# Kernel optimization log

Hardware: AMD Instinct MI355X
Metric: run time of the kernel (lower is better)

The kernel has to match this reference:

```python
import jax, jax.numpy as jnp
import numpy as np

B = 4; E_PER = 100_000; E = B * E_PER
N_NODES = 50_000; N_REL = 500; D = 64; D_LG = 256
K_PER_VI = 20; S_VI = E // K_PER_VI          # 20000 sorted vi segments
S_VJ_PER = 5_000; S_VJ = B * S_VJ_PER        # 20000 unsorted vj segments
N_MEM = 131_072
INTERACT = ((0, 3), (0, 2, 3), (0, 4), (0, 2, 4), (1, 3), (1, 2, 3), (1, 4), (1, 2, 4))


def _build_edges():
    rng = np.random.default_rng(0)
    idx_vi = np.repeat(np.arange(S_VI), K_PER_VI)          # sorted segment ids
    gpb = S_VI // B
    eg = idx_vi // gpb                                     # sorted by eg_idx too
    vi = rng.integers(0, N_NODES, S_VI)[idx_vi]
    idx_vj = np.empty(E, dtype=np.int64)
    for b in range(B):
        loc = np.concatenate([np.arange(S_VJ_PER), rng.integers(0, S_VJ_PER, E_PER - S_VJ_PER)])
        rng.shuffle(loc)
        idx_vj[b * E_PER:(b + 1) * E_PER] = b * S_VJ_PER + loc  # every group non-empty
    vj = rng.integers(0, N_NODES, S_VJ)[idx_vj]            # consistent (eg, vj) per group
    rel = rng.integers(0, N_REL, E)
    e2vi = rng.integers(0, N_MEM, E)
    e2vj = rng.integers(0, N_MEM, E)
    return np.stack([eg, vi, vj, rel, idx_vi, idx_vj, e2vi, e2vj], axis=1).astype(np.int32)


def setup_inputs() -> dict:
    key = jax.random.key(0)
    ks = jax.random.split(key, 10)
    return {
        "node_attention": jax.random.uniform(ks[0], (B, N_NODES), jnp.float32),
        "scanned_edges": jnp.asarray(_build_edges()),
        "edges_y": jax.random.uniform(ks[1], (E,), jnp.float32),
        "hidden_uncon": jax.random.normal(ks[2], (1, N_NODES, D_LG), jnp.float32),
        "hidden_con": jax.random.normal(ks[3], (N_MEM, D), jnp.float32),
        "Wc": jax.random.normal(ks[4], (D, D), jnp.float32) / np.sqrt(D).astype(np.float32),
        "bc": jnp.zeros((D,), jnp.float32),
        "Wu": jax.random.normal(ks[5], (D_LG, D), jnp.float32) / np.sqrt(D_LG).astype(np.float32),
        "bu": jnp.zeros((D,), jnp.float32),
        "rel_table": jax.random.normal(ks[6], (N_REL, D), jnp.float32) * 0.05,
        "ws": jax.random.normal(ks[7], (len(INTERACT), D), jnp.float32) / np.sqrt(float(len(INTERACT))).astype(np.float32) if False else jax.random.normal(ks[7], (len(INTERACT), D), jnp.float32) * (1.0 / np.sqrt(len(INTERACT)).astype(np.float32)),
        "fb": jnp.zeros((D,), jnp.float32),
        "out_w": jax.random.normal(ks[8], (D,), jnp.float32),
        "out_b": jnp.zeros((D,), jnp.float32),
        "n_vi_segments": S_VI,
        "n_vj_segments": S_VJ,
    }


def reference(node_attention, scanned_edges, edges_y, hidden_uncon, hidden_con,
              Wc, bc, Wu, bu, rel_table, ws, fb, out_w, out_b,
              n_vi_segments, n_vj_segments):
    eg, vi, vj, rel = (scanned_edges[:, i] for i in range(4))
    idx_vi, idx_vj, e2vi, e2vj = (scanned_edges[:, i] for i in range(4, 8))
    # projections (proj_con / proj_uncon, tanh Dense)
    hc = jnp.tanh(hidden_con @ Wc + bc)          # [N_MEM, D]
    hu = jnp.tanh(hidden_uncon @ Wu + bu)[0]     # [n_nodes, D]; batch_size==1 path of Node2Edge
    # Node2Edge gathers
    feats = (hc[e2vi], hu[vi], rel_table[rel], hc[e2vj], hu[vj])  # each [E, D]
    # F layer: weighted sum of elementwise interaction products
    out = fb
    for k, idxs in enumerate(INTERACT):
        x = feats[idxs[0]]
        for i in idxs[1:]:
            x = x * feats[i]
        out = out + x * ws[k]
    out = jax.nn.relu(out) * out_w + out_b
    logits = jnp.sum(out, axis=1)                # [E]
    # NeighborSoftmax at 'vi' (sorted segment softmax)
    m = jax.ops.segment_max(logits, idx_vi, num_segments=n_vi_segments)
    ex = jnp.exp(logits - m[idx_vi])
    den = jax.ops.segment_sum(ex, idx_vi, num_segments=n_vi_segments)
    transition = ex / den[idx_vi]
    # attention flow: gather source attention, weight, aggregate at vj
    trans_att = transition * node_attention[eg, vi] * edges_y
    aggr = jax.ops.segment_sum(trans_att, idx_vj, num_segments=n_vj_segments)
    b_g = jax.ops.segment_max(eg, idx_vj, num_segments=n_vj_segments)
    vj_g = jax.ops.segment_max(vj, idx_vj, num_segments=n_vj_segments)
    new_node_attention = jnp.zeros_like(node_attention).at[b_g, vj_g].add(aggr)
    return new_node_attention
```

## Files before the change

### kernel.cpp

```cpp
#include <hip/hip_runtime.h>
#include <hip/hip_bf16.h>
#include <type_traits>

#define D 64
#define KPER 20

typedef __attribute__((ext_vector_type(8))) short short8;
typedef __attribute__((ext_vector_type(4))) float floatx4;

__device__ __forceinline__ unsigned short f2bfu(float x) {
    __hip_bfloat16 h = __float2bfloat16(x);
    return *reinterpret_cast<unsigned short*>(&h);
}
__device__ __forceinline__ float bfu2f(unsigned short u) {
    return __uint_as_float(((unsigned)u) << 16);
}

__device__ __forceinline__ float fast_tanh(float x) {
    float xc = fminf(fmaxf(x, -15.f), 15.f);
    float e = __expf(2.f * xc);
    return 1.f - 2.f * __builtin_amdgcn_rcpf(1.f + e);
}

template<int CTRL>
__device__ __forceinline__ float dpp_add(float x) {
    int t = __builtin_amdgcn_update_dpp(0, __float_as_int(x), CTRL, 0xf, 0xf, true);
    return x + __int_as_float(t);
}
template<int CTRL>
__device__ __forceinline__ float dpp_max(float x) {
    int xi = __float_as_int(x);
    int t = __builtin_amdgcn_update_dpp(xi, xi, CTRL, 0xf, 0xf, false);
    return fmaxf(x, __int_as_float(t));
}
__device__ __forceinline__ float wave_sum_b(float x) {
    x = dpp_add<0x111>(x); x = dpp_add<0x112>(x);
    x = dpp_add<0x114>(x); x = dpp_add<0x118>(x);
    x = dpp_add<0x142>(x); x = dpp_add<0x143>(x);
    return __int_as_float(__builtin_amdgcn_readlane(__float_as_int(x), 63));
}
__device__ __forceinline__ float wave_max_b(float x) {
    x = dpp_max<0x111>(x); x = dpp_max<0x112>(x);
    x = dpp_max<0x114>(x); x = dpp_max<0x118>(x);
    x = dpp_max<0x142>(x); x = dpp_max<0x143>(x);
    return __int_as_float(__builtin_amdgcn_readlane(__float_as_int(x), 63));
}

template<int I, int N, typename F>
__device__ __forceinline__ void static_for(F&& f) {
    if constexpr (I < N) {
        f(std::integral_constant<int, I>{});
        static_for<I + 1, N>(f);
    }
}

template<int SLOT>
__device__ __forceinline__ int get_slot(int m0, int m1, int m2) {
    if constexpr (SLOT < 64)       return __builtin_amdgcn_readlane(m0, SLOT);
    else if constexpr (SLOT < 128) return __builtin_amdgcn_readlane(m1, SLOT - 64);
    else                           return __builtin_amdgcn_readlane(m2, SLOT - 128);
}

__device__ __forceinline__ void proj64_pair(const float* __restrict__ h,
        const float* __restrict__ W, const float* __restrict__ b,
        unsigned short* __restrict__ out, int rt0) {
    constexpr int K = 64, KT = 2, CTN = 4;
    int lane = threadIdx.x & 63;
    int m = lane & 15, quad = lane >> 4;
    short8 bfr[CTN][KT];
    #pragma unroll
    for (int ct = 0; ct < CTN; ++ct)
        #pragma unroll
        for (int kt = 0; kt < KT; ++kt)
            #pragma unroll
            for (int j = 0; j < 8; ++j)
                bfr[ct][kt][j] = (short)f2bfu(W[(size_t)(kt * 32 + quad * 8 + j) * 64 + ct * 16 + m]);
    float bv[CTN];
    #pragma unroll
    for (int ct = 0; ct < CTN; ++ct) bv[ct] = b[ct * 16 + m];
    int rt1 = rt0 + 1;
    const float* hrow0 = h + (size_t)(rt0 * 16 + m) * K + quad * 8;
    const float* hrow1 = h + (size_t)(rt1 * 16 + m) * K + quad * 8;
    floatx4 a0[KT][2], a1[KT][2];
    #pragma unroll
    for (int kt = 0; kt < KT; ++kt) {
        a0[kt][0] = *(const floatx4*)(hrow0 + kt * 32);
        a0[kt][1] = *(const floatx4*)(hrow0 + kt * 32 + 4);
        a1[kt][0] = *(const floatx4*)(hrow1 + kt * 32);
        a1[kt][1] = *(const floatx4*)(hrow1 + kt * 32 + 4);
    }
    #pragma unroll
    for (int t = 0; t < 2; ++t) {
        floatx4 (*ar)[2] = t ? a1 : a0;
        int rt = t ? rt1 : rt0;
        floatx4 acc[CTN];
        #pragma unroll
        for (int ct = 0; ct < CTN; ++ct) acc[ct] = floatx4{0.f, 0.f, 0.f, 0.f};
        #pragma unroll
        for (int kt = 0; kt < KT; ++kt) {
            short8 af;
            #pragma unroll
            for (int j = 0; j < 4; ++j) {
                af[j]     = (short)f2bfu(ar[kt][0][j]);
                af[j + 4] = (short)f2bfu(ar[kt][1][j]);
            }
            #pragma unroll
            for (int ct = 0; ct < CTN; ++ct)
                acc[ct] = __builtin_amdgcn_mfma_f32_16x16x32_bf16(af, bfr[ct][kt], acc[ct], 0, 0, 0);
        }
        #pragma unroll
        for (int ct = 0; ct < CTN; ++ct) {
            int col = ct * 16 + m;
            #pragma unroll
            for (int reg = 0; reg < 4; ++reg) {
                int row = rt * 16 + quad * 4 + reg;
                out[(size_t)row * 64 + col] = f2bfu(fast_tanh(acc[ct][reg] + bv[ct]));
            }
        }
    }
}

__device__ __forceinline__ void proj256_body(const float* __restrict__ h,
        const float* __restrict__ W, const float* __restrict__ b,
        unsigned short* __restrict__ out, int ct0, int rt0, int rtstride, int ntiles) {
    constexpr int K = 256, KT = 8, CTN = 2;
    int lane = threadIdx.x & 63;
    int m = lane & 15, quad = lane >> 4;
    short8 bfr[CTN][KT];
    #pragma unroll
    for (int ct = 0; ct < CTN; ++ct)
        #pragma unroll
        for (int kt = 0; kt < KT; ++kt)
            #pragma unroll
            for (int j = 0; j < 8; ++j)
                bfr[ct][kt][j] = (short)f2bfu(W[(size_t)(kt * 32 + quad * 8 + j) * 64 + (ct0 + ct) * 16 + m]);
    float bv[CTN];
    #pragma unroll
    for (int ct = 0; ct < CTN; ++ct) bv[ct] = b[(ct0 + ct) * 16 + m];
    for (int rt = rt0; rt < ntiles; rt += rtstride) {
        floatx4 acc[CTN];
        #pragma unroll
        for (int ct = 0; ct < CTN; ++ct) acc[ct] = floatx4{0.f, 0.f, 0.f, 0.f};
        const float* hrow = h + (size_t)(rt * 16 + m) * K + quad * 8;
        #pragma unroll
        for (int kt = 0; kt < KT; ++kt) {
            floatx4 v0 = *(const floatx4*)(hrow + kt * 32);
            floatx4 v1 = *(const floatx4*)(hrow + kt * 32 + 4);
            short8 af;
            #pragma unroll
            for (int j = 0; j < 4; ++j) {
                af[j]     = (short)f2bfu(v0[j]);
                af[j + 4] = (short)f2bfu(v1[j]);
            }
            #pragma unroll
            for (int ct = 0; ct < CTN; ++ct)
                acc[ct] = __builtin_amdgcn_mfma_f32_16x16x32_bf16(af, bfr[ct][kt], acc[ct], 0, 0, 0);
        }
        #pragma unroll
        for (int ct = 0; ct < CTN; ++ct) {
            int col = (ct0 + ct) * 16 + m;
            #pragma unroll
            for (int reg = 0; reg < 4; ++reg) {
                int row = rt * 16 + quad * 4 + reg;
                out[(size_t)row * 64 + col] = f2bfu(fast_tanh(acc[ct][reg] + bv[ct]));
            }
        }
    }
}

#define RELB 16
#define ZB 8
__global__ __launch_bounds__(256) void proj_fused(
        const float* __restrict__ hcon, const float* __restrict__ Wc, const float* __restrict__ bc,
        const float* __restrict__ hun, const float* __restrict__ Wu, const float* __restrict__ bu,
        const float* __restrict__ relf, unsigned short* __restrict__ hc,
        unsigned short* __restrict__ hu, unsigned short* __restrict__ relb,
        float* __restrict__ outz, int nout,
        int t64, int t256, int g64, int g256, int nrel) {
    int bid = blockIdx.x;
    int w = threadIdx.x >> 6;
    if (bid < g64) {
        int wid = bid * 4 + w;
        proj64_pair(hcon, Wc, bc, hc, wid * 2);
    } else if (bid < g64 + g256) {
        int wid = (bid - g64) * 4 + w;
        int half = wid & 1;
        proj256_body(hun, Wu, bu, hu, half * 2, wid >> 1, (g256 * 4) >> 1, t256);
    } else if (bid < g64 + g256 + RELB) {
        int tid = (bid - g64 - g256) * 256 + threadIdx.x;
        for (int i = tid; i < nrel; i += RELB * 256) relb[i] = f2bfu(relf[i]);
    } else {
        int tid = (bid - g64 - g256 - RELB) * 256 + threadIdx.x;
        for (int i = tid; i < nout; i += ZB * 256) outz[i] = 0.0f;
    }
}

__global__ __launch_bounds__(256) void edge_kernel(
        const float* __restrict__ natt, const int* __restrict__ edges,
        const float* __restrict__ ey, const unsigned short* __restrict__ hc,
        const unsigned short* __restrict__ hu, const unsigned short* __restrict__ relt,
        const float* __restrict__ wsm, const float* __restrict__ fb,
        const float* __restrict__ outw, float* __restrict__ out, int N) {
    int lane = threadIdx.x & 63;
    int s = blockIdx.x * 4 + (threadIdx.x >> 6);
    long base = (long)s * KPER;
    const int* eb = edges + base * 8;
    int m0 = eb[lane];
    int m1 = eb[64 + lane];
    int m2 = (lane < 32) ? eb[128 + lane] : 0;
    int eg = get_slot<0>(m0, m1, m2);
    int vi = get_slot<1>(m0, m1, m2);
    float f1 = bfu2f(hu[(size_t)vi * D + lane]);
    float na = natt[(size_t)eg * N + vi];
    float w0 = wsm[0 * D + lane], w1 = wsm[1 * D + lane];
    float w2 = wsm[2 * D + lane], w3 = wsm[3 * D + lane];
    float w4 = wsm[4 * D + lane], w5 = wsm[5 * D + lane];
    float w6 = wsm[6 * D + lane], w7 = wsm[7 * D + lane];
    float fbv = fb[lane], owv = outw[lane];
    float myl = -INFINITY;
    int myvj = 0;
    static_for<0, KPER>([&](auto ec) {
        constexpr int e = decltype(ec)::value;
        int vj  = get_slot<e * 8 + 2>(m0, m1, m2);
        int rel = get_slot<e * 8 + 3>(m0, m1, m2);
        int evi = get_slot<e * 8 + 6>(m0, m1, m2);
        int evj = get_slot<e * 8 + 7>(m0, m1, m2);
        float F0 = bfu2f(hc[(size_t)evi * D + lane]);
        float F2 = bfu2f(relt[(size_t)rel * D + lane]);
        float F3 = bfu2f(hc[(size_t)evj * D + lane]);
        float F4 = bfu2f(hu[(size_t)vj * D + lane]);
        float t1 = fmaf(F2, w1, w0);
        float t2 = fmaf(F2, w5, w4);
        float t3 = fmaf(F2, w3, w2);
        float t4 = fmaf(F2, w7, w6);
        float u = fmaf(F0, t1, f1 * t2);
        float v = fmaf(F0, t3, f1 * t4);
        float o = fmaf(F3, u, fmaf(F4, v, fbv));
        o = fmaxf(o, 0.0f) * owv;
        float tot = wave_sum_b(o);
        bool mine = (lane == e);
        myl = mine ? tot : myl;
        myvj = mine ? vj : myvj;
    });
    float mx = wave_max_b(myl);
    float ex = __expf(myl - mx);
    float den = wave_sum_b(ex);
    if (lane < KPER) {
        float t = (ex / den) * na * ey[base + lane];
        atomicAdd(out + (size_t)eg * N + myvj, t);
    }
}

extern "C" void kernel_launch(void* const* d_in, const int* in_sizes, int n_in,
                              void* d_out, int out_size, void* d_ws, size_t ws_size,
                              hipStream_t stream) {
    const float* natt = (const float*)d_in[0];
    const int*   edges = (const int*)d_in[1];
    const float* ey   = (const float*)d_in[2];
    const float* hun  = (const float*)d_in[3];
    const float* hcon = (const float*)d_in[4];
    const float* Wc   = (const float*)d_in[5];
    const float* bc   = (const float*)d_in[6];
    const float* Wu   = (const float*)d_in[7];
    const float* bu   = (const float*)d_in[8];
    const float* relt = (const float*)d_in[9];
    const float* wsm  = (const float*)d_in[10];
    const float* fb   = (const float*)d_in[11];
    const float* outw = (const float*)d_in[12];
    float* out = (float*)d_out;

    int E    = in_sizes[2];
    int S    = E / KPER;
    int nmem = in_sizes[4] / D;
    int N    = in_sizes[3] / 256;
    int nrel = in_sizes[9];

    int t64  = nmem / 16;
    int t256 = N / 16;
    int g64  = t64 / 8;
    int g256 = 512;

    unsigned short* hc = (unsigned short*)d_ws;
    unsigned short* hu = hc + (size_t)nmem * D;
    unsigned short* rb = hu + (size_t)N * D;

    proj_fused<<<g64 + g256 + RELB + ZB, 256, 0, stream>>>(hcon, Wc, bc, hun, Wu, bu,
                                                           relt, hc, hu, rb,
                                                           out, out_size,
                                                           t64, t256, g64, g256, nrel);
    edge_kernel<<<S / 4, 256, 0, stream>>>(natt, edges, ey, hc, hu, rb,
                                           wsm, fb, outw, out, N);
}
```

Measured before the change: 209.2 us.

## Prefetch all edge gathers before compute and widen projection work per wave

The edge kernel now issues all 80 bf16 gathers for a segment's 20 edges up front into register arrays, before the compute and reduction loop. This exposes more memory-level parallelism instead of relying on the compiler to interleave loads with the cross-lane reductions. The 64-wide projection now does four row tiles per wave instead of two, and the 256-wide projection makes each wave cover all four column tiles rather than half. Both changes cut redundant weight loading and conversion, at the cost of higher register pressure and possibly lower occupancy.

```diff
diff --git a/kernel.cpp b/kernel.cpp
--- a/kernel.cpp
+++ b/kernel.cpp
@@ -61,10 +61,10 @@
     else                           return __builtin_amdgcn_readlane(m2, SLOT - 128);
 }
 
-__device__ __forceinline__ void proj64_pair(const float* __restrict__ h,
+__device__ __forceinline__ void proj64_quad(const float* __restrict__ h,
         const float* __restrict__ W, const float* __restrict__ b,
         unsigned short* __restrict__ out, int rt0) {
-    constexpr int K = 64, KT = 2, CTN = 4;
+    constexpr int K = 64, KT = 2, CTN = 4, NT = 4;
     int lane = threadIdx.x & 63;
     int m = lane & 15, quad = lane >> 4;
     short8 bfr[CTN][KT];
@@ -78,21 +78,19 @@
     float bv[CTN];
     #pragma unroll
     for (int ct = 0; ct < CTN; ++ct) bv[ct] = b[ct * 16 + m];
-    int rt1 = rt0 + 1;
-    const float* hrow0 = h + (size_t)(rt0 * 16 + m) * K + quad * 8;
-    const float* hrow1 = h + (size_t)(rt1 * 16 + m) * K + quad * 8;
-    floatx4 a0[KT][2], a1[KT][2];
-    #pragma unroll
-    for (int kt = 0; kt < KT; ++kt) {
-        a0[kt][0] = *(const floatx4*)(hrow0 + kt * 32);
-        a0[kt][1] = *(const floatx4*)(hrow0 + kt * 32 + 4);
-        a1[kt][0] = *(const floatx4*)(hrow1 + kt * 32);
-        a1[kt][1] = *(const floatx4*)(hrow1 + kt * 32 + 4);
-    }
-    #pragma unroll
-    for (int t = 0; t < 2; ++t) {
-        floatx4 (*ar)[2] = t ? a1 : a0;
-        int rt = t ? rt1 : rt0;
+    floatx4 a[NT][KT][2];
+    #pragma unroll
+    for (int t = 0; t < NT; ++t) {
+        const float* hrow = h + (size_t)((rt0 + t) * 16 + m) * K + quad * 8;
+        #pragma unroll
+        for (int kt = 0; kt < KT; ++kt) {
+            a[t][kt][0] = *(const floatx4*)(hrow + kt * 32);
+            a[t][kt][1] = *(const floatx4*)(hrow + kt * 32 + 4);
+        }
+    }
+    #pragma unroll
+    for (int t = 0; t < NT; ++t) {
+        int rt = rt0 + t;
         floatx4 acc[CTN];
         #pragma unroll
         for (int ct = 0; ct < CTN; ++ct) acc[ct] = floatx4{0.f, 0.f, 0.f, 0.f};
@@ -101,8 +99,8 @@
             short8 af;
             #pragma unroll
             for (int j = 0; j < 4; ++j) {
-                af[j]     = (short)f2bfu(ar[kt][0][j]);
-                af[j + 4] = (short)f2bfu(ar[kt][1][j]);
+                af[j]     = (short)f2bfu(a[t][kt][0][j]);
+                af[j + 4] = (short)f2bfu(a[t][kt][1][j]);
             }
             #pragma unroll
             for (int ct = 0; ct < CTN; ++ct)
@@ -120,10 +118,10 @@
     }
 }
 
-__device__ __forceinline__ void proj256_body(const float* __restrict__ h,
+__device__ __forceinline__ void proj256_full(const float* __restrict__ h,
         const float* __restrict__ W, const float* __restrict__ b,
-        unsigned short* __restrict__ out, int ct0, int rt0, int rtstride, int ntiles) {
-    constexpr int K = 256, KT = 8, CTN = 2;
+        unsigned short* __restrict__ out, int rt0, int rtstride, int ntiles) {
+    constexpr int K = 256, KT = 8, CTN = 4;
     int lane = threadIdx.x & 63;
     int m = lane & 15, quad = lane >> 4;
     short8 bfr[CTN][KT];
@@ -133,10 +131,10 @@
         for (int kt = 0; kt < KT; ++kt)
             #pragma unroll
             for (int j = 0; j < 8; ++j)
-                bfr[ct][kt][j] = (short)f2bfu(W[(size_t)(kt * 32 + quad * 8 + j) * 64 + (ct0 + ct) * 16 + m]);
+                bfr[ct][kt][j] = (short)f2bfu(W[(size_t)(kt * 32 + quad * 8 + j) * 64 + ct * 16 + m]);
     float bv[CTN];
     #pragma unroll
-    for (int ct = 0; ct < CTN; ++ct) bv[ct] = b[(ct0 + ct) * 16 + m];
+    for (int ct = 0; ct < CTN; ++ct) bv[ct] = b[ct * 16 + m];
     for (int rt = rt0; rt < ntiles; rt += rtstride) {
         floatx4 acc[CTN];
         #pragma unroll
@@ -158,7 +156,7 @@
         }
         #pragma unroll
         for (int ct = 0; ct < CTN; ++ct) {
-            int col = (ct0 + ct) * 16 + m;
+            int col = ct * 16 + m;
             #pragma unroll
             for (int reg = 0; reg < 4; ++reg) {
                 int row = rt * 16 + quad * 4 + reg;
@@ -181,11 +179,10 @@
     int w = threadIdx.x >> 6;
     if (bid < g64) {
         int wid = bid * 4 + w;
-        proj64_pair(hcon, Wc, bc, hc, wid * 2);
+        proj64_quad(hcon, Wc, bc, hc, wid * 4);
     } else if (bid < g64 + g256) {
         int wid = (bid - g64) * 4 + w;
-        int half = wid & 1;
-        proj256_body(hun, Wu, bu, hu, half * 2, wid >> 1, (g256 * 4) >> 1, t256);
+        proj256_full(hun, Wu, bu, hu, wid, g256 * 4, t256);
     } else if (bid < g64 + g256 + RELB) {
         int tid = (bid - g64 - g256) * 256 + threadIdx.x;
         for (int i = tid; i < nrel; i += RELB * 256) relb[i] = f2bfu(relf[i]);
@@ -212,6 +209,22 @@
     int vi = get_slot<1>(m0, m1, m2);
     float f1 = bfu2f(hu[(size_t)vi * D + lane]);
     float na = natt[(size_t)eg * N + vi];
+
+    unsigned short F0r[KPER], F2r[KPER], F3r[KPER], F4r[KPER];
+    int vjr[KPER];
+    static_for<0, KPER>([&](auto ec) {
+        constexpr int e = decltype(ec)::value;
+        int vj  = get_slot<e * 8 + 2>(m0, m1, m2);
+        int rel = get_slot<e * 8 + 3>(m0, m1, m2);
+        int evi = get_slot<e * 8 + 6>(m0, m1, m2);
+        int evj = get_slot<e * 8 + 7>(m0, m1, m2);
+        F0r[e] = hc[(size_t)evi * D + lane];
+        F2r[e] = relt[(size_t)rel * D + lane];
+        F3r[e] = hc[(size_t)evj * D + lane];
+        F4r[e] = hu[(size_t)vj * D + lane];
+        vjr[e] = vj;
+    });
+
     float w0 = wsm[0 * D + lane], w1 = wsm[1 * D + lane];
     float w2 = wsm[2 * D + lane], w3 = wsm[3 * D + lane];
     float w4 = wsm[4 * D + lane], w5 = wsm[5 * D + lane];
@@ -221,14 +234,10 @@
     int myvj = 0;
     static_for<0, KPER>([&](auto ec) {
         constexpr int e = decltype(ec)::value;
-        int vj  = get_slot<e * 8 + 2>(m0, m1, m2);
-        int rel = get_slot<e * 8 + 3>(m0, m1, m2);
-        int evi = get_slot<e * 8 + 6>(m0, m1, m2);
-        int evj = get_slot<e * 8 + 7>(m0, m1, m2);
-        float F0 = bfu2f(hc[(size_t)evi * D + lane]);
-        float F2 = bfu2f(relt[(size_t)rel * D + lane]);
-        float F3 = bfu2f(hc[(size_t)evj * D + lane]);
-        float F4 = bfu2f(hu[(size_t)vj * D + lane]);
+        float F0 = bfu2f(F0r[e]);
+        float F2 = bfu2f(F2r[e]);
+        float F3 = bfu2f(F3r[e]);
+        float F4 = bfu2f(F4r[e]);
         float t1 = fmaf(F2, w1, w0);
         float t2 = fmaf(F2, w5, w4);
         float t3 = fmaf(F2, w3, w2);
@@ -240,7 +249,7 @@
         float tot = wave_sum_b(o);
         bool mine = (lane == e);
         myl = mine ? tot : myl;
-        myvj = mine ? vj : myvj;
+        myvj = mine ? vjr[e] : myvj;
     });
     float mx = wave_max_b(myl);
     float ex = __expf(myl - mx);
@@ -277,7 +286,7 @@
 
     int t64  = nmem / 16;
     int t256 = N / 16;
-    int g64  = t64 / 8;
+    int g64  = t64 / 16;
     int g256 = 512;
 
     unsigned short* hc = (unsigned short*)d_ws;
```

Result: faster. 204.5 us (-2.2%).

## Process four edges per wave with vectorized bf16 gathers issued up front

Applied to the files above, without the earlier changes.

The edge kernel now splits each wave into four 16-lane groups. Each group handles one edge per iteration, with each lane owning 4 features loaded as a uint2 (4 bf16 values). All 20 edges' index loads and feature gathers are issued before any compute, which raises memory-level parallelism. Per-edge reductions shrink from 20 full-wave DPP reductions to 5 row-of-16 reductions plus a shuffle, and the per-edge readlane index extraction is replaced by direct per-group loads. The cost is higher register pressure from holding all gathered data at once.

```diff
diff --git a/kernel.cpp b/kernel.cpp
--- a/kernel.cpp
+++ b/kernel.cpp
@@ -45,20 +45,10 @@
     x = dpp_max<0x142>(x); x = dpp_max<0x143>(x);
     return __int_as_float(__builtin_amdgcn_readlane(__float_as_int(x), 63));
 }
-
-template<int I, int N, typename F>
-__device__ __forceinline__ void static_for(F&& f) {
-    if constexpr (I < N) {
-        f(std::integral_constant<int, I>{});
-        static_for<I + 1, N>(f);
-    }
-}
-
-template<int SLOT>
-__device__ __forceinline__ int get_slot(int m0, int m1, int m2) {
-    if constexpr (SLOT < 64)       return __builtin_amdgcn_readlane(m0, SLOT);
-    else if constexpr (SLOT < 128) return __builtin_amdgcn_readlane(m1, SLOT - 64);
-    else                           return __builtin_amdgcn_readlane(m2, SLOT - 128);
+__device__ __forceinline__ float row16_sum(float x) {
+    x = dpp_add<0x111>(x); x = dpp_add<0x112>(x);
+    x = dpp_add<0x114>(x); x = dpp_add<0x118>(x);
+    return x;
 }
 
 __device__ __forceinline__ void proj64_pair(const float* __restrict__ h,
@@ -195,6 +185,13 @@
     }
 }
 
+__device__ __forceinline__ void unp4(uint2 u, float f[4]) {
+    f[0] = __uint_as_float(u.x << 16);
+    f[1] = __uint_as_float(u.x & 0xffff0000u);
+    f[2] = __uint_as_float(u.y << 16);
+    f[3] = __uint_as_float(u.y & 0xffff0000u);
+}
+
 __global__ __launch_bounds__(256) void edge_kernel(
         const float* __restrict__ natt, const int* __restrict__ edges,
         const float* __restrict__ ey, const unsigned short* __restrict__ hc,
@@ -202,50 +199,68 @@
         const float* __restrict__ wsm, const float* __restrict__ fb,
         const float* __restrict__ outw, float* __restrict__ out, int N) {
     int lane = threadIdx.x & 63;
+    int g = lane >> 4, sub = lane & 15;
+    int l2 = lane >> 2;
     int s = blockIdx.x * 4 + (threadIdx.x >> 6);
     long base = (long)s * KPER;
     const int* eb = edges + base * 8;
-    int m0 = eb[lane];
-    int m1 = eb[64 + lane];
-    int m2 = (lane < 32) ? eb[128 + lane] : 0;
-    int eg = get_slot<0>(m0, m1, m2);
-    int vi = get_slot<1>(m0, m1, m2);
-    float f1 = bfu2f(hu[(size_t)vi * D + lane]);
+    int eg = __builtin_amdgcn_readfirstlane(eb[0]);
+    int vi = __builtin_amdgcn_readfirstlane(eb[1]);
+
+    const int* ebg = eb + g * 8;
+    int vjx[5], relx[5], evix[5], evjx[5];
+    #pragma unroll
+    for (int i = 0; i < 5; ++i) {
+        vjx[i]  = ebg[i * 32 + 2];
+        relx[i] = ebg[i * 32 + 3];
+        evix[i] = ebg[i * 32 + 6];
+        evjx[i] = ebg[i * 32 + 7];
+    }
+    uint2 G0[5], G2[5], G3[5], G4[5];
+    #pragma unroll
+    for (int i = 0; i < 5; ++i) {
+        G0[i] = *(const uint2*)(hc   + (size_t)evix[i] * D + sub * 4);
+        G2[i] = *(const uint2*)(relt + (size_t)relx[i] * D + sub * 4);
+        G3[i] = *(const uint2*)(hc   + (size_t)evjx[i] * D + sub * 4);
+        G4[i] = *(const uint2*)(hu   + (size_t)vjx[i]  * D + sub * 4);
+    }
+    uint2 F1u = *(const uint2*)(hu + (size_t)vi * D + sub * 4);
+    float f1[4];
+    unp4(F1u, f1);
+
+    floatx4 wv[8];
+    #pragma unroll
+    for (int k = 0; k < 8; ++k) wv[k] = *(const floatx4*)(wsm + k * D + sub * 4);
+    floatx4 fbv = *(const floatx4*)(fb + sub * 4);
+    floatx4 owv = *(const floatx4*)(outw + sub * 4);
     float na = natt[(size_t)eg * N + vi];
-    float w0 = wsm[0 * D + lane], w1 = wsm[1 * D + lane];
-    float w2 = wsm[2 * D + lane], w3 = wsm[3 * D + lane];
-    float w4 = wsm[4 * D + lane], w5 = wsm[5 * D + lane];
-    float w6 = wsm[6 * D + lane], w7 = wsm[7 * D + lane];
-    float fbv = fb[lane], owv = outw[lane];
+
     float myl = -INFINITY;
-    int myvj = 0;
-    static_for<0, KPER>([&](auto ec) {
-        constexpr int e = decltype(ec)::value;
-        int vj  = get_slot<e * 8 + 2>(m0, m1, m2);
-        int rel = get_slot<e * 8 + 3>(m0, m1, m2);
-        int evi = get_slot<e * 8 + 6>(m0, m1, m2);
-        int evj = get_slot<e * 8 + 7>(m0, m1, m2);
-        float F0 = bfu2f(hc[(size_t)evi * D + lane]);
-        float F2 = bfu2f(relt[(size_t)rel * D + lane]);
-        float F3 = bfu2f(hc[(size_t)evj * D + lane]);
-        float F4 = bfu2f(hu[(size_t)vj * D + lane]);
-        float t1 = fmaf(F2, w1, w0);
-        float t2 = fmaf(F2, w5, w4);
-        float t3 = fmaf(F2, w3, w2);
-        float t4 = fmaf(F2, w7, w6);
-        float u = fmaf(F0, t1, f1 * t2);
-        float v = fmaf(F0, t3, f1 * t4);
-        float o = fmaf(F3, u, fmaf(F4, v, fbv));
-        o = fmaxf(o, 0.0f) * owv;
-        float tot = wave_sum_b(o);
-        bool mine = (lane == e);
-        myl = mine ? tot : myl;
-        myvj = mine ? vj : myvj;
-    });
+    #pragma unroll
+    for (int i = 0; i < 5; ++i) {
+        float F0[4], F2[4], F3[4], F4[4];
+        unp4(G0[i], F0); unp4(G2[i], F2); unp4(G3[i], F3); unp4(G4[i], F4);
+        float acc = 0.f;
+        #pragma unroll
+        for (int j = 0; j < 4; ++j) {
+            float t1 = fmaf(F2[j], wv[1][j], wv[0][j]);
+            float t2 = fmaf(F2[j], wv[5][j], wv[4][j]);
+            float t3 = fmaf(F2[j], wv[3][j], wv[2][j]);
+            float t4 = fmaf(F2[j], wv[7][j], wv[6][j]);
+            float u = fmaf(F0[j], t1, f1[j] * t2);
+            float v = fmaf(F0[j], t3, f1[j] * t4);
+            float od = fmaf(F3[j], u, fmaf(F4[j], v, fbv[j]));
+            acc = fmaf(fmaxf(od, 0.f), owv[j], acc);
+        }
+        float rs = row16_sum(acc);
+        float tot = __shfl(rs, ((lane & 3) << 4) + 15);
+        myl = (l2 == i) ? tot : myl;
+    }
     float mx = wave_max_b(myl);
     float ex = __expf(myl - mx);
     float den = wave_sum_b(ex);
     if (lane < KPER) {
+        int myvj = eb[lane * 8 + 2];
         float t = (ex / den) * na * ey[base + lane];
         atomicAdd(out + (size_t)eg * N + myvj, t);
     }
```

New measurement: 203.6 us. 1.03x faster.
